# Optimization experiments

Measured on AMD Instinct MI355X. Metric: run time of the kernel, lower is better.

Reference implementation:

```python
import jax, jax.numpy as jnp
import numpy as np

B = 32768
STATE, BELIEF, HID, EMB, ACT = 100, 200, 200, 1024, 32
MIN_STD = 0.1

def _dense_init(key, fan_in, fan_out):
    k1, k2 = jax.random.split(key)
    scale = 1.0 / np.sqrt(fan_in)
    W = jax.random.uniform(k1, (fan_in, fan_out), jnp.float32, -scale, scale)
    b = jnp.zeros((fan_out,), jnp.float32)
    return W, b

def setup_inputs() -> dict:
    key = jax.random.key(0)
    ks = jax.random.split(key, 20)
    inp = {
        'prev_state': jax.random.normal(ks[0], (1, B, STATE), jnp.float32),
        'prev_action': jax.random.normal(ks[1], (1, B, ACT), jnp.float32),
        'prev_belief': jax.random.normal(ks[2], (1, B, BELIEF), jnp.float32),
        'observation': jax.random.normal(ks[3], (1, B, EMB), jnp.float32),
        'nonterminals': jnp.ones((1, B, 1), jnp.float32),
    }
    # fc_embed_state_action: (state+action) -> belief_dim, relu
    inp['W_sa'], inp['b_sa'] = _dense_init(ks[4], STATE + ACT, BELIEF)
    # GRUCell: carry = hidden (belief_dim), inputs = prev_belief (belief_dim)
    inp['W_ir'], inp['b_ir'] = _dense_init(ks[5], BELIEF, BELIEF)
    inp['W_iz'], inp['b_iz'] = _dense_init(ks[6], BELIEF, BELIEF)
    inp['W_in'], inp['b_in'] = _dense_init(ks[7], BELIEF, BELIEF)
    inp['W_hr'], _ = _dense_init(ks[8], BELIEF, BELIEF)   # no bias (flax GRUCell)
    inp['W_hz'], _ = _dense_init(ks[9], BELIEF, BELIEF)   # no bias
    inp['W_hn'], inp['b_hn'] = _dense_init(ks[10], BELIEF, BELIEF)
    # prior head
    inp['W_bp'], inp['b_bp'] = _dense_init(ks[11], BELIEF, HID)
    inp['W_sp'], inp['b_sp'] = _dense_init(ks[12], HID, 2 * STATE)
    # posterior head
    inp['W_bq'], inp['b_bq'] = _dense_init(ks[13], BELIEF + EMB, HID)
    inp['W_sq'], inp['b_sq'] = _dense_init(ks[14], HID, 2 * STATE)
    return inp

def reference(prev_state, prev_action, prev_belief, observation, nonterminals,
              W_sa, b_sa, W_ir, b_ir, W_iz, b_iz, W_in, b_in,
              W_hr, W_hz, W_hn, b_hn,
              W_bp, b_bp, W_sp, b_sp, W_bq, b_bq, W_sq, b_sq):
    noise_key = jax.random.key(42)  # stands in for the module's fixed self.rng
    s = prev_state * nonterminals  # broadcast mask over last dim
    # fc_embed_state_action (relu, activate_final=True)
    h = jax.nn.relu(jnp.concatenate([s, prev_action], axis=-1) @ W_sa + b_sa)
    # flax GRUCell with carry = h, inputs = prev_belief
    x = prev_belief
    r = jax.nn.sigmoid(x @ W_ir + b_ir + h @ W_hr)
    z = jax.nn.sigmoid(x @ W_iz + b_iz + h @ W_hz)
    n = jnp.tanh(x @ W_in + b_in + r * (h @ W_hn + b_hn))
    new_belief = (1.0 - z) * n + z * h
    # prior
    hp = jax.nn.relu(new_belief @ W_bp + b_bp)
    prior_out = jax.nn.relu(hp @ W_sp + b_sp)  # activate_final=True
    prior_mean, prior_std_raw = jnp.split(prior_out, 2, axis=-1)
    prior_std = jax.nn.softplus(prior_std_raw) + MIN_STD
    eps = jax.random.normal(noise_key, prior_mean.shape, prior_mean.dtype)
    prior_state = prior_mean + prior_std * eps
    # posterior
    hq = jax.nn.relu(jnp.concatenate([new_belief, observation], axis=-1) @ W_bq + b_bq)
    post_out = jax.nn.relu(hq @ W_sq + b_sq)
    post_mean, post_std_raw = jnp.split(post_out, 2, axis=-1)
    post_std = jax.nn.softplus(post_std_raw) + MIN_STD
    eps2 = jax.random.normal(noise_key, post_mean.shape, post_mean.dtype)  # same rng reused, as in source
    post_state = post_mean + post_std * eps2
    return (new_belief, prior_state, prior_mean, prior_std, post_state, post_mean, post_std)
```

## Files before the change

### kernel.cpp

```cpp
#include <hip/hip_runtime.h>
#include <stdint.h>

typedef short short8 __attribute__((ext_vector_type(8)));
typedef float floatx4 __attribute__((ext_vector_type(4)));
typedef unsigned short ushort_t;

#define BATCH 32768
#define STR   232
#define SLAB  (16*STR)
#define TOT_TILES 1391

#define M_SA 0
#define M_IR 1
#define M_HR 2
#define M_IZ 3
#define M_HZ 4
#define M_IN 5
#define M_HN 6
#define M_BP 7
#define M_SP 8
#define M_SQ 9
#define M_BQ 10

__device__ constexpr int TILE0[11] = {0,65,156,247,338,429,520,611,702,793,884};
__device__ constexpr int KLIM[11]  = {132,200,200,200,200,200,200,200,200,200,0};

__device__ __forceinline__ ushort_t f2bf(float f){
  uint32_t u = __float_as_uint(f);
  uint32_t r = (u + 0x7fffu + ((u >> 16) & 1u)) >> 16;
  return (ushort_t)r;
}
__device__ __forceinline__ float bf2f(ushort_t h){ return __uint_as_float(((uint32_t)h) << 16); }

__device__ __forceinline__ float sigmf_(float x){ return 1.f / (1.f + expf(-x)); }
__device__ __forceinline__ float softplusf_(float x){
  return fmaxf(x, 0.f) + log1pf(expf(-fabsf(x)));
}
__device__ __forceinline__ uint32_t rotl32(uint32_t x, int r){ return (x << r) | (x >> (32 - r)); }

__device__ __forceinline__ void threefry2x32_k42(uint32_t x0, uint32_t x1,
                                                 uint32_t& o0, uint32_t& o1){
  const uint32_t k0 = 0u, k1 = 42u, k2 = 0u ^ 42u ^ 0x1BD11BDAu;
  x0 += k0; x1 += k1;
#define TF_R(rot) { x0 += x1; x1 = rotl32(x1, rot); x1 ^= x0; }
  TF_R(13) TF_R(15) TF_R(26) TF_R(6)  x0 += k1; x1 += k2 + 1u;
  TF_R(17) TF_R(29) TF_R(16) TF_R(24) x0 += k2; x1 += k0 + 2u;
  TF_R(13) TF_R(15) TF_R(26) TF_R(6)  x0 += k0; x1 += k1 + 3u;
  TF_R(17) TF_R(29) TF_R(16) TF_R(24) x0 += k1; x1 += k2 + 4u;
  TF_R(13) TF_R(15) TF_R(26) TF_R(6)  x0 += k2; x1 += k0 + 5u;
#undef TF_R
  o0 = x0; o1 = x1;
}

__device__ __forceinline__ float jax_erfinv(float x){
  float w = -log1pf(-x * x);
  float p;
  if (w < 5.0f) {
    w -= 2.5f;
    p = 2.81022636e-08f;
    p = fmaf(p, w, 3.43273939e-07f);
    p = fmaf(p, w, -3.5233877e-06f);
    p = fmaf(p, w, -4.39150654e-06f);
    p = fmaf(p, w, 0.00021858087f);
    p = fmaf(p, w, -0.00125372503f);
    p = fmaf(p, w, -0.00417768164f);
    p = fmaf(p, w, 0.246640727f);
    p = fmaf(p, w, 1.50140941f);
  } else {
    w = sqrtf(w) - 3.0f;
    p = -0.000200214257f;
    p = fmaf(p, w, 0.000100950558f);
    p = fmaf(p, w, 0.00134934322f);
    p = fmaf(p, w, -0.00367342844f);
    p = fmaf(p, w, 0.00573950773f);
    p = fmaf(p, w, -0.0076224613f);
    p = fmaf(p, w, 0.00943887047f);
    p = fmaf(p, w, 1.00167406f);
    p = fmaf(p, w, 2.83297682f);
  }
  return p * x;
}

__device__ __forceinline__ float jax_normal_at(uint32_t j){
  uint32_t o0, o1;
  threefry2x32_k42(0u, j, o0, o1);
  uint32_t bits = o0 ^ o1;
  const float lo = -0.99999994f;
  float f = __uint_as_float((bits >> 9) | 0x3f800000u) - 1.0f;
  float fm = f * 1.99999994f;
  float u = fmaxf(lo, fm + lo);
  return 1.41421356f * jax_erfinv(u);
}

struct ConvP { const float* src[11]; ushort_t* dst; };

__global__ void __launch_bounds__(64) convw(ConvP cp)
{
  int t = blockIdx.x;
  int lane = threadIdx.x;
  const int cum[12] = {0,65,156,247,338,429,520,611,702,793,884,1391};
  int mi = 0;
  #pragma unroll
  for (int i = 0; i < 11; ++i) if (t >= cum[i+1]) mi = i+1;
  int lt = t - cum[mi];
  int kb = lt / 13, nt = lt - kb*13;
  const float* S = cp.src[mi];
  int q = lane >> 4, m = lane & 15;
  int n = nt*16 + m;
  ushort_t* D = cp.dst + (size_t)t*512 + lane*8;
  #pragma unroll
  for (int j = 0; j < 8; ++j){
    int k = kb*32 + q*8 + j;
    float v = 0.f;
    if (n < 200){
      if (mi == 10){
        if (k < 200) v = S[k*200+n];
        else if (k >= 224) v = S[(size_t)(k-24)*200+n];
      } else {
        int K = (mi == 0) ? 132 : 200;
        if (k < K) v = S[k*200+n];
      }
    }
    D[j] = f2bf(v);
  }
}

struct MainP {
  const float* prev_state; const float* prev_action; const float* prev_belief;
  const float* observation; const float* nonterm;
  const float* b_sa; const float* b_ir; const float* b_iz; const float* b_in; const float* b_hn;
  const float* b_bp; const float* b_sp; const float* b_bq; const float* b_sq;
  const float* W[11];
  const ushort_t* ws;
  float* out;
};

__device__ __forceinline__ short8 afrag(const ushort_t* buf, int m, int kb, int q){
  return *(const short8*)(buf + m*STR + kb*32 + q*8);
}

#define NSTEPS 214
#define STAGE_US 3584

struct Sched {
  short t0[NSTEPS]; signed char cnt[NSTEPS];
  constexpr Sched() : t0(), cnt() {
    int s = 0;
    for (int kb = 0; kb < 5; ++kb){
      t0[s] = (short)(0 + kb*13);     cnt[s] = 7; ++s;
      t0[s] = (short)(0 + kb*13 + 7); cnt[s] = 6; ++s;
    }
    for (int kb = 0; kb < 7; ++kb)
      for (int mt = 1; mt <= 6; ++mt){ t0[s] = (short)(65 + 91*(mt-1) + kb*13);     cnt[s] = 7; ++s; }
    for (int kb = 0; kb < 7; ++kb)
      for (int mt = 1; mt <= 6; ++mt){ t0[s] = (short)(65 + 91*(mt-1) + kb*13 + 7); cnt[s] = 6; ++s; }
    for (int kb = 0; kb < 7; ++kb){
      t0[s] = (short)(611 + kb*13);     cnt[s] = 7; ++s;
      t0[s] = (short)(611 + kb*13 + 7); cnt[s] = 6; ++s;
    }
    for (int kb = 0; kb < 7; ++kb){
      t0[s] = (short)(702 + kb*13);     cnt[s] = 7; ++s;
      t0[s] = (short)(702 + kb*13 + 7); cnt[s] = 6; ++s;
    }
    for (int kb = 0; kb < 39; ++kb){
      t0[s] = (short)(884 + kb*13);     cnt[s] = 7; ++s;
      t0[s] = (short)(884 + kb*13 + 7); cnt[s] = 6; ++s;
    }
    for (int kb = 0; kb < 7; ++kb){
      t0[s] = (short)(793 + kb*13);     cnt[s] = 7; ++s;
      t0[s] = (short)(793 + kb*13 + 7); cnt[s] = 6; ++s;
    }
  }
};
__device__ constexpr Sched SCHED{};

__device__ __forceinline__ void stage_issue(const ushort_t* ws, ushort_t* sbuf,
                                            int step, int w, int lane)
{
  if (step >= NSTEPS) return;
  const int t0 = SCHED.t0[step];
  const int cn = SCHED.cnt[step];
  ushort_t* dstb = sbuf + (step & 1) * STAGE_US;
  const ushort_t* srcb = ws + ((size_t)t0 << 9) + (lane << 3);
  #pragma unroll
  for (int r = 0; r < 2; ++r){
    int tt = w + r*4;
    if (tt < cn){
      __builtin_amdgcn_global_load_lds(
        (const __attribute__((address_space(1))) uint32_t*)(const void*)(srcb + (tt << 9)),
        (__attribute__((address_space(3)))       uint32_t*)(void*)(dstb + (tt << 9)),
        16, 0, 0);
    }
  }
}

__device__ __forceinline__ short8 sfrag(const ushort_t* sbuf, int step, int j, int lane){
  return *(const short8*)(sbuf + (step & 1) * STAGE_US + (j << 9) + (lane << 3));
}

__device__ __forceinline__ void gemm13_kb(const MainP& p, ushort_t* stageb, int& sidx,
    const ushort_t* asrc, floatx4 (&acc)[13], int kb, int m, int q, int lane, int w)
{
  short8 a = afrag(asrc, m, kb, q);
  stage_issue(p.ws, stageb, sidx+1, w, lane);
  #pragma unroll
  for (int j = 0; j < 7; ++j)
    acc[j] = __builtin_amdgcn_mfma_f32_16x16x32_bf16(a, sfrag(stageb, sidx, j, lane), acc[j], 0,0,0);
  __syncthreads(); ++sidx;
  stage_issue(p.ws, stageb, sidx+1, w, lane);
  #pragma unroll
  for (int j = 0; j < 6; ++j)
    acc[7+j] = __builtin_amdgcn_mfma_f32_16x16x32_bf16(a, sfrag(stageb, sidx, j, lane), acc[7+j], 0,0,0);
  __syncthreads(); ++sidx;
}

template<int CNT, int NT0>
__device__ __forceinline__ void gru_chunk_staged(const MainP& p, ushort_t* stageb, int& sidx,
    const ushort_t* bufX, const ushort_t* bufH, int R0, int m, int q, int lane, int w,
    floatx4 (&nbv)[13])
{
  floatx4 aR[CNT], aZ[CNT], aXN[CNT], aHN[CNT];
  #pragma unroll
  for (int i = 0; i < CNT; ++i){
    int col = (NT0+i)*16 + m;
    float br = (col<200)? p.b_ir[col] : 0.f;
    float bz = (col<200)? p.b_iz[col] : 0.f;
    float bn = (col<200)? p.b_in[col] : 0.f;
    float bh = (col<200)? p.b_hn[col] : 0.f;
    aR[i]  = (floatx4){br,br,br,br};
    aZ[i]  = (floatx4){bz,bz,bz,bz};
    aXN[i] = (floatx4){bn,bn,bn,bn};
    aHN[i] = (floatx4){bh,bh,bh,bh};
  }
#define GRU_STEP(AV, ACC) \
  stage_issue(p.ws, stageb, sidx+1, w, lane); \
  _Pragma("unroll") \
  for (int i = 0; i < CNT; ++i) \
    ACC[i] = __builtin_amdgcn_mfma_f32_16x16x32_bf16(AV, sfrag(stageb, sidx, i, lane), ACC[i], 0,0,0); \
  __syncthreads(); ++sidx;

  #pragma unroll 1
  for (int kb = 0; kb < 7; ++kb){
    short8 ax = afrag(bufX, m, kb, q);
    short8 ah = afrag(bufH, m, kb, q);
    GRU_STEP(ax, aR)
    GRU_STEP(ah, aR)
    GRU_STEP(ax, aZ)
    GRU_STEP(ah, aZ)
    GRU_STEP(ax, aXN)
    GRU_STEP(ah, aHN)
  }
#undef GRU_STEP
  #pragma unroll
  for (int i = 0; i < CNT; ++i){
    int col = (NT0+i)*16 + m;
    if (col < 200){
      #pragma unroll
      for (int rg = 0; rg < 4; ++rg){
        int rowl = q*4 + rg;
        float rr = sigmf_(aR[i][rg]);
        float zz = sigmf_(aZ[i][rg]);
        float nn = tanhf(fmaf(rr, aHN[i][rg], aXN[i][rg]));
        float hv = bf2f(bufH[rowl*STR + col]);
        float nb = fmaf(zz, hv - nn, nn);
        nbv[NT0+i][rg] = nb;
        __builtin_nontemporal_store(nb, &p.out[(size_t)(R0+rowl)*200 + col]);
      }
    }
  }
}

__device__ __forceinline__ void head_out(const floatx4* acc, float* sdb,
    float* o_state, float* o_mean, float* o_std, int R0, int m, int q)
{
  #pragma unroll
  for (int nt = 6; nt < 13; ++nt){
    int col = nt*16 + m;
    if (col >= 100 && col < 200){
      #pragma unroll
      for (int rg = 0; rg < 4; ++rg){
        int rowl = q*4 + rg;
        float sr = fmaxf(acc[nt][rg], 0.f);
        float sd = softplusf_(sr) + 0.1f;
        sdb[rowl*100 + (col-100)] = sd;
        __builtin_nontemporal_store(sd, &o_std[(size_t)(R0+rowl)*100 + (col-100)]);
      }
    }
  }
  __syncthreads();
  #pragma unroll
  for (int nt = 0; nt < 7; ++nt){
    int col = nt*16 + m;
    if (col < 100){
      #pragma unroll
      for (int rg = 0; rg < 4; ++rg){
        int rowl = q*4 + rg;
        float mean = fmaxf(acc[nt][rg], 0.f);
        float sd = sdb[rowl*100 + col];
        float e = jax_normal_at((uint32_t)(R0+rowl)*100u + (uint32_t)col);
        __builtin_nontemporal_store(mean, &o_mean[(size_t)(R0+rowl)*100 + col]);
        __builtin_nontemporal_store(fmaf(sd, e, mean), &o_state[(size_t)(R0+rowl)*100 + col]);
      }
    }
  }
  __syncthreads();
}

__global__ void __launch_bounds__(256, 2) rssm_staged(MainP p)
{
  __shared__ __align__(16) ushort_t lds[8*SLAB + 2*STAGE_US];

  const int tid  = threadIdx.x;
  const int w    = tid >> 6;
  const int lane = tid & 63;
  const int q    = lane >> 4;
  const int m    = lane & 15;
  const int R0   = blockIdx.x * 64 + w * 16;

  ushort_t* bufX   = lds + w * 2 * SLAB;
  ushort_t* bufH   = bufX + SLAB;
  ushort_t* stageb = lds + 8*SLAB;
  int sidx = 0;

  stage_issue(p.ws, stageb, 0, w, lane);

  for (int t = lane; t < 16*160; t += 64){
    int rr = t / 160, cc = t - rr*160;
    int grow = R0 + rr;
    float v = 0.f;
    if (cc < 100)      v = p.prev_state[(size_t)grow*100 + cc] * p.nonterm[grow];
    else if (cc < 132) v = p.prev_action[(size_t)grow*32 + (cc-100)];
    bufX[rr*STR + cc] = f2bf(v);
  }
  for (int t = lane; t < 16*24; t += 64){
    int rr = t / 24, cc = 200 + (t - rr*24);
    bufH[rr*STR + cc] = 0;
  }
  __syncthreads();

  {
    floatx4 acc[13];
    #pragma unroll
    for (int nt = 0; nt < 13; ++nt){
      int col = nt*16 + m;
      float bv = (col<200)? p.b_sa[col] : 0.f;
      acc[nt] = (floatx4){bv,bv,bv,bv};
    }
    #pragma unroll 1
    for (int kb = 0; kb < 5; ++kb)
      gemm13_kb(p, stageb, sidx, bufX, acc, kb, m, q, lane, w);
    #pragma unroll
    for (int nt = 0; nt < 13; ++nt){
      int col = nt*16 + m;
      if (col < 200){
        #pragma unroll
        for (int rg = 0; rg < 4; ++rg)
          bufH[(q*4+rg)*STR + col] = f2bf(fmaxf(acc[nt][rg], 0.f));
      }
    }
  }

  for (int t = lane; t < 16*224; t += 64){
    int rr = t / 224, cc = t - rr*224;
    float v = 0.f;
    if (cc < 200)
      v = __builtin_nontemporal_load(&p.prev_belief[(size_t)(R0+rr)*200 + cc]);
    bufX[rr*STR + cc] = f2bf(v);
  }
  __syncthreads();

  floatx4 nbv[13];
  gru_chunk_staged<7,0>(p, stageb, sidx, bufX, bufH, R0, m, q, lane, w, nbv);
  gru_chunk_staged<6,7>(p, stageb, sidx, bufX, bufH, R0, m, q, lane, w, nbv);

  #pragma unroll
  for (int nt = 0; nt < 13; ++nt){
    int col = nt*16 + m;
    if (col < 200){
      #pragma unroll
      for (int rg = 0; rg < 4; ++rg)
        bufX[(q*4+rg)*STR + col] = f2bf(nbv[nt][rg]);
    }
  }

  {
    floatx4 acc[13];
    #pragma unroll
    for (int nt = 0; nt < 13; ++nt){
      int col = nt*16 + m;
      float bv = (col<200)? p.b_bp[col] : 0.f;
      acc[nt] = (floatx4){bv,bv,bv,bv};
    }
    #pragma unroll 1
    for (int kb = 0; kb < 7; ++kb)
      gemm13_kb(p, stageb, sidx, bufX, acc, kb, m, q, lane, w);
    #pragma unroll
    for (int nt = 0; nt < 13; ++nt){
      int col = nt*16 + m;
      if (col < 200){
        #pragma unroll
        for (int rg = 0; rg < 4; ++rg)
          bufH[(q*4+rg)*STR + col] = f2bf(fmaxf(acc[nt][rg], 0.f));
      }
    }
  }
  __syncthreads();

  {
    floatx4 acc[13];
    #pragma unroll
    for (int nt = 0; nt < 13; ++nt){
      int col = nt*16 + m;
      float bv = (col<200)? p.b_sp[col] : 0.f;
      acc[nt] = (floatx4){bv,bv,bv,bv};
    }
    #pragma unroll 1
    for (int kb = 0; kb < 7; ++kb)
      gemm13_kb(p, stageb, sidx, bufH, acc, kb, m, q, lane, w);
    head_out(acc, (float*)bufH,
             p.out + (size_t)BATCH*200, p.out + (size_t)BATCH*300, p.out + (size_t)BATCH*400,
             R0, m, q);
  }

  {
    floatx4 acc[13];
    #pragma unroll
    for (int nt = 0; nt < 13; ++nt){
      int col = nt*16 + m;
      float bv = (col<200)? p.b_bq[col] : 0.f;
      acc[nt] = (floatx4){bv,bv,bv,bv};
    }
    #pragma unroll 1
    for (int kb = 0; kb < 7; ++kb)
      gemm13_kb(p, stageb, sidx, bufX, acc, kb, m, q, lane, w);

    const float* orow_base = p.observation + (size_t)(R0+m)*1024;
    floatx4 o1 = __builtin_nontemporal_load((const floatx4*)(orow_base + 0 + q*8));
    floatx4 o2 = __builtin_nontemporal_load((const floatx4*)(orow_base + 0 + q*8 + 4));
    #pragma unroll 1
    for (int kb = 7; kb < 39; ++kb){
      floatx4 n1 = {0,0,0,0}, n2 = {0,0,0,0};
      if (kb < 38){
        const float* nr = orow_base + ((kb+1)*32 - 224) + q*8;
        n1 = __builtin_nontemporal_load((const floatx4*)(nr));
        n2 = __builtin_nontemporal_load((const floatx4*)(nr + 4));
      }
      short8 ao;
      ao[0] = (short)f2bf(o1[0]); ao[1] = (short)f2bf(o1[1]);
      ao[2] = (short)f2bf(o1[2]); ao[3] = (short)f2bf(o1[3]);
      ao[4] = (short)f2bf(o2[0]); ao[5] = (short)f2bf(o2[1]);
      ao[6] = (short)f2bf(o2[2]); ao[7] = (short)f2bf(o2[3]);
      stage_issue(p.ws, stageb, sidx+1, w, lane);
      #pragma unroll
      for (int j = 0; j < 7; ++j)
        acc[j] = __builtin_amdgcn_mfma_f32_16x16x32_bf16(ao, sfrag(stageb, sidx, j, lane), acc[j], 0,0,0);
      __syncthreads(); ++sidx;
      stage_issue(p.ws, stageb, sidx+1, w, lane);
      #pragma unroll
      for (int j = 0; j < 6; ++j)
        acc[7+j] = __builtin_amdgcn_mfma_f32_16x16x32_bf16(ao, sfrag(stageb, sidx, j, lane), acc[7+j], 0,0,0);
      __syncthreads(); ++sidx;
      o1 = n1; o2 = n2;
    }
    #pragma unroll
    for (int nt = 0; nt < 13; ++nt){
      int col = nt*16 + m;
      if (col < 200){
        #pragma unroll
        for (int rg = 0; rg < 4; ++rg)
          bufH[(q*4+rg)*STR + col] = f2bf(fmaxf(acc[nt][rg], 0.f));
      }
    }
    for (int t = lane; t < 16*24; t += 64){
      int rr = t / 24, cc = 200 + (t - rr*24);
      bufH[rr*STR + cc] = 0;
    }
  }
  __syncthreads();

  {
    floatx4 acc[13];
    #pragma unroll
    for (int nt = 0; nt < 13; ++nt){
      int col = nt*16 + m;
      float bv = (col<200)? p.b_sq[col] : 0.f;
      acc[nt] = (floatx4){bv,bv,bv,bv};
    }
    #pragma unroll 1
    for (int kb = 0; kb < 7; ++kb)
      gemm13_kb(p, stageb, sidx, bufH, acc, kb, m, q, lane, w);
    head_out(acc, (float*)bufX,
             p.out + (size_t)BATCH*500, p.out + (size_t)BATCH*600, p.out + (size_t)BATCH*700,
             R0, m, q);
  }
}

template<int MAT>
__device__ __forceinline__ short8 bfr0(const MainP& p, int kb, int nt, int lane, int q, int m){
  int n = nt*16 + m;
  const float* S = p.W[MAT];
  uint32_t u[8];
  #pragma unroll
  for (int j = 0; j < 8; ++j){
    int k = kb*32 + q*8 + j;
    int srow;
    if (MAT == M_BQ) srow = (k < 200) ? k : ((k >= 224) ? k - 24 : -1);
    else             srow = (k < KLIM[MAT]) ? k : -1;
    float v = (srow >= 0 && n < 200) ? S[(size_t)srow*200 + n] : 0.f;
    u[j] = __float_as_uint(v);
  }
  short8 r;
  #pragma unroll
  for (int j = 0; j < 8; ++j) r[j] = (short)(u[j] >> 16);
  return r;
}

template<int CNT, int NT0>
__device__ __forceinline__ void gru_chunk0(const MainP& p,
    const ushort_t* bufX, const ushort_t* bufH, int R0, int m, int q, int lane,
    floatx4 (&nbv)[13])
{
  floatx4 aR[CNT], aZ[CNT], aXN[CNT], aHN[CNT];
  #pragma unroll
  for (int i = 0; i < CNT; ++i){
    int col = (NT0+i)*16 + m;
    float br = (col<200)? p.b_ir[col] : 0.f;
    float bz = (col<200)? p.b_iz[col] : 0.f;
    float bn = (col<200)? p.b_in[col] : 0.f;
    float bh = (col<200)? p.b_hn[col] : 0.f;
    aR[i]  = (floatx4){br,br,br,br};
    aZ[i]  = (floatx4){bz,bz,bz,bz};
    aXN[i] = (floatx4){bn,bn,bn,bn};
    aHN[i] = (floatx4){bh,bh,bh,bh};
  }
  #pragma unroll 1
  for (int kb = 0; kb < 7; ++kb){
    short8 ax = afrag(bufX, m, kb, q);
    short8 ah = afrag(bufH, m, kb, q);
    #pragma unroll
    for (int i = 0; i < CNT; ++i){
      int nt = NT0 + i;
      aR[i]  = __builtin_amdgcn_mfma_f32_16x16x32_bf16(ax, bfr0<M_IR>(p,kb,nt,lane,q,m), aR[i], 0,0,0);
      aR[i]  = __builtin_amdgcn_mfma_f32_16x16x32_bf16(ah, bfr0<M_HR>(p,kb,nt,lane,q,m), aR[i], 0,0,0);
      aZ[i]  = __builtin_amdgcn_mfma_f32_16x16x32_bf16(ax, bfr0<M_IZ>(p,kb,nt,lane,q,m), aZ[i], 0,0,0);
      aZ[i]  = __builtin_amdgcn_mfma_f32_16x16x32_bf16(ah, bfr0<M_HZ>(p,kb,nt,lane,q,m), aZ[i], 0,0,0);
      aXN[i] = __builtin_amdgcn_mfma_f32_16x16x32_bf16(ax, bfr0<M_IN>(p,kb,nt,lane,q,m), aXN[i], 0,0,0);
      aHN[i] = __builtin_amdgcn_mfma_f32_16x16x32_bf16(ah, bfr0<M_HN>(p,kb,nt,lane,q,m), aHN[i], 0,0,0);
    }
  }
  #pragma unroll
  for (int i = 0; i < CNT; ++i){
    int col = (NT0+i)*16 + m;
    if (col < 200){
      #pragma unroll
      for (int rg = 0; rg < 4; ++rg){
        int rowl = q*4 + rg;
        float rr = sigmf_(aR[i][rg]);
        float zz = sigmf_(aZ[i][rg]);
        float nn = tanhf(fmaf(rr, aHN[i][rg], aXN[i][rg]));
        float hv = bf2f(bufH[rowl*STR + col]);
        float nb = fmaf(zz, hv - nn, nn);
        nbv[NT0+i][rg] = nb;
        __builtin_nontemporal_store(nb, &p.out[(size_t)(R0+rowl)*200 + col]);
      }
    }
  }
}

__global__ void __launch_bounds__(256, 2) rssm_direct(MainP p)
{
  __shared__ __align__(16) ushort_t lds[4 * 2 * SLAB];

  const int tid  = threadIdx.x;
  const int w    = tid >> 6;
  const int lane = tid & 63;
  const int q    = lane >> 4;
  const int m    = lane & 15;
  const int R0   = blockIdx.x * 64 + w * 16;

  ushort_t* bufX = lds + w * 2 * SLAB;
  ushort_t* bufH = bufX + SLAB;

  for (int t = lane; t < 16*160; t += 64){
    int rr = t / 160, cc = t - rr*160;
    int grow = R0 + rr;
    float v = 0.f;
    if (cc < 100)      v = p.prev_state[(size_t)grow*100 + cc] * p.nonterm[grow];
    else if (cc < 132) v = p.prev_action[(size_t)grow*32 + (cc-100)];
    bufX[rr*STR + cc] = f2bf(v);
  }
  for (int t = lane; t < 16*24; t += 64){
    int rr = t / 24, cc = 200 + (t - rr*24);
    bufH[rr*STR + cc] = 0;
  }
  __syncthreads();

  {
    floatx4 acc[13];
    #pragma unroll
    for (int nt = 0; nt < 13; ++nt){
      int col = nt*16 + m;
      float bv = (col<200)? p.b_sa[col] : 0.f;
      acc[nt] = (floatx4){bv,bv,bv,bv};
    }
    #pragma unroll 1
    for (int kb = 0; kb < 5; ++kb){
      short8 a = afrag(bufX, m, kb, q);
      #pragma unroll
      for (int nt = 0; nt < 13; ++nt)
        acc[nt] = __builtin_amdgcn_mfma_f32_16x16x32_bf16(a, bfr0<M_SA>(p,kb,nt,lane,q,m), acc[nt], 0,0,0);
    }
    #pragma unroll
    for (int nt = 0; nt < 13; ++nt){
      int col = nt*16 + m;
      if (col < 200){
        #pragma unroll
        for (int rg = 0; rg < 4; ++rg)
          bufH[(q*4+rg)*STR + col] = f2bf(fmaxf(acc[nt][rg], 0.f));
      }
    }
  }

  for (int t = lane; t < 16*224; t += 64){
    int rr = t / 224, cc = t - rr*224;
    float v = 0.f;
    if (cc < 200)
      v = __builtin_nontemporal_load(&p.prev_belief[(size_t)(R0+rr)*200 + cc]);
    bufX[rr*STR + cc] = f2bf(v);
  }
  __syncthreads();

  floatx4 nbv[13];
  gru_chunk0<7,0>(p, bufX, bufH, R0, m, q, lane, nbv);
  gru_chunk0<6,7>(p, bufX, bufH, R0, m, q, lane, nbv);

  #pragma unroll
  for (int nt = 0; nt < 13; ++nt){
    int col = nt*16 + m;
    if (col < 200){
      #pragma unroll
      for (int rg = 0; rg < 4; ++rg)
        bufX[(q*4+rg)*STR + col] = f2bf(nbv[nt][rg]);
    }
  }

  {
    floatx4 acc[13];
    #pragma unroll
    for (int nt = 0; nt < 13; ++nt){
      int col = nt*16 + m;
      float bv = (col<200)? p.b_bp[col] : 0.f;
      acc[nt] = (floatx4){bv,bv,bv,bv};
    }
    #pragma unroll 1
    for (int kb = 0; kb < 7; ++kb){
      short8 a = afrag(bufX, m, kb, q);
      #pragma unroll
      for (int nt = 0; nt < 13; ++nt)
        acc[nt] = __builtin_amdgcn_mfma_f32_16x16x32_bf16(a, bfr0<M_BP>(p,kb,nt,lane,q,m), acc[nt], 0,0,0);
    }
    #pragma unroll
    for (int nt = 0; nt < 13; ++nt){
      int col = nt*16 + m;
      if (col < 200){
        #pragma unroll
        for (int rg = 0; rg < 4; ++rg)
          bufH[(q*4+rg)*STR + col] = f2bf(fmaxf(acc[nt][rg], 0.f));
      }
    }
  }
  __syncthreads();

  {
    floatx4 acc[13];
    #pragma unroll
    for (int nt = 0; nt < 13; ++nt){
      int col = nt*16 + m;
      float bv = (col<200)? p.b_sp[col] : 0.f;
      acc[nt] = (floatx4){bv,bv,bv,bv};
    }
    #pragma unroll 1
    for (int kb = 0; kb < 7; ++kb){
      short8 a = afrag(bufH, m, kb, q);
      #pragma unroll
      for (int nt = 0; nt < 13; ++nt)
        acc[nt] = __builtin_amdgcn_mfma_f32_16x16x32_bf16(a, bfr0<M_SP>(p,kb,nt,lane,q,m), acc[nt], 0,0,0);
    }
    head_out(acc, (float*)bufH,
             p.out + (size_t)BATCH*200, p.out + (size_t)BATCH*300, p.out + (size_t)BATCH*400,
             R0, m, q);
  }

  {
    floatx4 acc[13];
    #pragma unroll
    for (int nt = 0; nt < 13; ++nt){
      int col = nt*16 + m;
      float bv = (col<200)? p.b_bq[col] : 0.f;
      acc[nt] = (floatx4){bv,bv,bv,bv};
    }
    #pragma unroll 1
    for (int kb = 0; kb < 7; ++kb){
      short8 a = afrag(bufX, m, kb, q);
      #pragma unroll
      for (int nt = 0; nt < 13; ++nt)
        acc[nt] = __builtin_amdgcn_mfma_f32_16x16x32_bf16(a, bfr0<M_BQ>(p,kb,nt,lane,q,m), acc[nt], 0,0,0);
    }
    const float* orow_base = p.observation + (size_t)(R0+m)*1024;
    #pragma unroll 1
    for (int kb = 7; kb < 39; ++kb){
      const float* orow = orow_base + (kb*32 - 224) + q*8;
      floatx4 o1 = __builtin_nontemporal_load((const floatx4*)(orow));
      floatx4 o2 = __builtin_nontemporal_load((const floatx4*)(orow + 4));
      short8 ao;
      ao[0] = (short)f2bf(o1[0]); ao[1] = (short)f2bf(o1[1]);
      ao[2] = (short)f2bf(o1[2]); ao[3] = (short)f2bf(o1[3]);
      ao[4] = (short)f2bf(o2[0]); ao[5] = (short)f2bf(o2[1]);
      ao[6] = (short)f2bf(o2[2]); ao[7] = (short)f2bf(o2[3]);
      #pragma unroll
      for (int nt = 0; nt < 13; ++nt)
        acc[nt] = __builtin_amdgcn_mfma_f32_16x16x32_bf16(ao, bfr0<M_BQ>(p,kb,nt,lane,q,m), acc[nt], 0,0,0);
    }
    #pragma unroll
    for (int nt = 0; nt < 13; ++nt){
      int col = nt*16 + m;
      if (col < 200){
        #pragma unroll
        for (int rg = 0; rg < 4; ++rg)
          bufH[(q*4+rg)*STR + col] = f2bf(fmaxf(acc[nt][rg], 0.f));
      }
    }
    for (int t = lane; t < 16*24; t += 64){
      int rr = t / 24, cc = 200 + (t - rr*24);
      bufH[rr*STR + cc] = 0;
    }
  }
  __syncthreads();

  {
    floatx4 acc[13];
    #pragma unroll
    for (int nt = 0; nt < 13; ++nt){
      int col = nt*16 + m;
      float bv = (col<200)? p.b_sq[col] : 0.f;
      acc[nt] = (floatx4){bv,bv,bv,bv};
    }
    #pragma unroll 1
    for (int kb = 0; kb < 7; ++kb){
      short8 a = afrag(bufH, m, kb, q);
      #pragma unroll
      for (int nt = 0; nt < 13; ++nt)
        acc[nt] = __builtin_amdgcn_mfma_f32_16x16x32_bf16(a, bfr0<M_SQ>(p,kb,nt,lane,q,m), acc[nt], 0,0,0);
    }
    head_out(acc, (float*)bufX,
             p.out + (size_t)BATCH*500, p.out + (size_t)BATCH*600, p.out + (size_t)BATCH*700,
             R0, m, q);
  }
}

extern "C" void kernel_launch(void* const* d_in, const int* in_sizes, int n_in,
                              void* d_out, int out_size, void* d_ws, size_t ws_size,
                              hipStream_t stream)
{
  MainP p;
  p.prev_state  = (const float*)d_in[0];
  p.prev_action = (const float*)d_in[1];
  p.prev_belief = (const float*)d_in[2];
  p.observation = (const float*)d_in[3];
  p.nonterm     = (const float*)d_in[4];
  p.b_sa = (const float*)d_in[6];
  p.b_ir = (const float*)d_in[8];
  p.b_iz = (const float*)d_in[10];
  p.b_in = (const float*)d_in[12];
  p.b_hn = (const float*)d_in[16];
  p.b_bp = (const float*)d_in[18];
  p.b_sp = (const float*)d_in[20];
  p.b_bq = (const float*)d_in[22];
  p.b_sq = (const float*)d_in[24];
  p.W[M_SA] = (const float*)d_in[5];
  p.W[M_IR] = (const float*)d_in[7];
  p.W[M_HR] = (const float*)d_in[13];
  p.W[M_IZ] = (const float*)d_in[9];
  p.W[M_HZ] = (const float*)d_in[14];
  p.W[M_IN] = (const float*)d_in[11];
  p.W[M_HN] = (const float*)d_in[15];
  p.W[M_BP] = (const float*)d_in[17];
  p.W[M_SP] = (const float*)d_in[19];
  p.W[M_SQ] = (const float*)d_in[23];
  p.W[M_BQ] = (const float*)d_in[21];
  p.ws   = (const ushort_t*)d_ws;
  p.out  = (float*)d_out;

  bool use_ws = (ws_size >= (size_t)TOT_TILES * 1024u);
  if (use_ws){
    ConvP cp;
    cp.src[0]  = p.W[M_SA]; cp.src[1]  = p.W[M_IR]; cp.src[2]  = p.W[M_HR];
    cp.src[3]  = p.W[M_IZ]; cp.src[4]  = p.W[M_HZ]; cp.src[5]  = p.W[M_IN];
    cp.src[6]  = p.W[M_HN]; cp.src[7]  = p.W[M_BP]; cp.src[8]  = p.W[M_SP];
    cp.src[9]  = p.W[M_SQ]; cp.src[10] = p.W[M_BQ];
    cp.dst     = (ushort_t*)d_ws;
    convw<<<TOT_TILES, 64, 0, stream>>>(cp);
    rssm_staged<<<512, 256, 0, stream>>>(p);
  } else {
    rssm_direct<<<512, 256, 0, stream>>>(p);
  }
}
```

Before: 525.5 us.

## Triple-buffer weight staging with partial vmcnt waits instead of full barriers

Moves the LDS weight staging ring from double to triple buffering, prefetching two steps ahead. Each full __syncthreads is replaced with an s_waitcnt vmcnt(N) that waits only for the oldest outstanding loads, followed by s_barrier, so newer prefetches and observation loads stay in flight. Several standalone barriers between phases are removed on the assumption that the next step_sync covers them. This grows LDS use, which may limit the two-blocks-per-CU occupancy, and relies on precise vmcnt accounting, so the removed barriers risk read/write races.

```diff
diff --git a/kernel.cpp b/kernel.cpp
--- a/kernel.cpp
+++ b/kernel.cpp
@@ -180,7 +180,7 @@
   if (step >= NSTEPS) return;
   const int t0 = SCHED.t0[step];
   const int cn = SCHED.cnt[step];
-  ushort_t* dstb = sbuf + (step & 1) * STAGE_US;
+  ushort_t* dstb = sbuf + (step % 3) * STAGE_US;
   const ushort_t* srcb = ws + ((size_t)t0 << 9) + (lane << 3);
   #pragma unroll
   for (int r = 0; r < 2; ++r){
@@ -195,23 +195,41 @@
 }
 
 __device__ __forceinline__ short8 sfrag(const ushort_t* sbuf, int step, int j, int lane){
-  return *(const short8*)(sbuf + (step & 1) * STAGE_US + (j << 9) + (lane << 3));
+  return *(const short8*)(sbuf + (step % 3) * STAGE_US + (j << 9) + (lane << 3));
+}
+
+__device__ __forceinline__ void step_sync(int sidx, int w, int extra)
+{
+  int n2 = 0;
+  if (sidx + 2 < NSTEPS){
+    int cn = SCHED.cnt[sidx + 2];
+    n2 = (w < cn ? 1 : 0) + ((w + 4) < cn ? 1 : 0);
+  }
+  int nw = n2 + extra;
+  switch (nw){
+    case 0:  asm volatile("s_waitcnt vmcnt(0)" ::: "memory"); break;
+    case 1:  asm volatile("s_waitcnt vmcnt(1)" ::: "memory"); break;
+    case 2:  asm volatile("s_waitcnt vmcnt(2)" ::: "memory"); break;
+    case 3:  asm volatile("s_waitcnt vmcnt(3)" ::: "memory"); break;
+    default: asm volatile("s_waitcnt vmcnt(4)" ::: "memory"); break;
+  }
+  __builtin_amdgcn_s_barrier();
 }
 
 __device__ __forceinline__ void gemm13_kb(const MainP& p, ushort_t* stageb, int& sidx,
     const ushort_t* asrc, floatx4 (&acc)[13], int kb, int m, int q, int lane, int w)
 {
   short8 a = afrag(asrc, m, kb, q);
-  stage_issue(p.ws, stageb, sidx+1, w, lane);
+  stage_issue(p.ws, stageb, sidx+2, w, lane);
   #pragma unroll
   for (int j = 0; j < 7; ++j)
     acc[j] = __builtin_amdgcn_mfma_f32_16x16x32_bf16(a, sfrag(stageb, sidx, j, lane), acc[j], 0,0,0);
-  __syncthreads(); ++sidx;
-  stage_issue(p.ws, stageb, sidx+1, w, lane);
+  step_sync(sidx, w, 0); ++sidx;
+  stage_issue(p.ws, stageb, sidx+2, w, lane);
   #pragma unroll
   for (int j = 0; j < 6; ++j)
     acc[7+j] = __builtin_amdgcn_mfma_f32_16x16x32_bf16(a, sfrag(stageb, sidx, j, lane), acc[7+j], 0,0,0);
-  __syncthreads(); ++sidx;
+  step_sync(sidx, w, 0); ++sidx;
 }
 
 template<int CNT, int NT0>
@@ -233,11 +251,11 @@
     aHN[i] = (floatx4){bh,bh,bh,bh};
   }
 #define GRU_STEP(AV, ACC) \
-  stage_issue(p.ws, stageb, sidx+1, w, lane); \
+  stage_issue(p.ws, stageb, sidx+2, w, lane); \
   _Pragma("unroll") \
   for (int i = 0; i < CNT; ++i) \
     ACC[i] = __builtin_amdgcn_mfma_f32_16x16x32_bf16(AV, sfrag(stageb, sidx, i, lane), ACC[i], 0,0,0); \
-  __syncthreads(); ++sidx;
+  step_sync(sidx, w, 0); ++sidx;
 
   #pragma unroll 1
   for (int kb = 0; kb < 7; ++kb){
@@ -287,7 +305,6 @@
       }
     }
   }
-  __syncthreads();
   #pragma unroll
   for (int nt = 0; nt < 7; ++nt){
     int col = nt*16 + m;
@@ -303,12 +320,11 @@
       }
     }
   }
-  __syncthreads();
 }
 
 __global__ void __launch_bounds__(256, 2) rssm_staged(MainP p)
 {
-  __shared__ __align__(16) ushort_t lds[8*SLAB + 2*STAGE_US];
+  __shared__ __align__(16) ushort_t lds[8*SLAB + 3*STAGE_US];
 
   const int tid  = threadIdx.x;
   const int w    = tid >> 6;
@@ -323,6 +339,7 @@
   int sidx = 0;
 
   stage_issue(p.ws, stageb, 0, w, lane);
+  stage_issue(p.ws, stageb, 1, w, lane);
 
   for (int t = lane; t < 16*160; t += 64){
     int rr = t / 160, cc = t - rr*160;
@@ -336,7 +353,8 @@
     int rr = t / 24, cc = 200 + (t - rr*24);
     bufH[rr*STR + cc] = 0;
   }
-  __syncthreads();
+  asm volatile("s_waitcnt vmcnt(0)" ::: "memory");
+  __builtin_amdgcn_s_barrier();
 
   {
     floatx4 acc[13];
@@ -367,7 +385,6 @@
       v = __builtin_nontemporal_load(&p.prev_belief[(size_t)(R0+rr)*200 + cc]);
     bufX[rr*STR + cc] = f2bf(v);
   }
-  __syncthreads();
 
   floatx4 nbv[13];
   gru_chunk_staged<7,0>(p, stageb, sidx, bufX, bufH, R0, m, q, lane, w, nbv);
@@ -404,7 +421,6 @@
       }
     }
   }
-  __syncthreads();
 
   {
     floatx4 acc[13];
@@ -435,32 +451,35 @@
       gemm13_kb(p, stageb, sidx, bufX, acc, kb, m, q, lane, w);
 
     const float* orow_base = p.observation + (size_t)(R0+m)*1024;
-    floatx4 o1 = __builtin_nontemporal_load((const floatx4*)(orow_base + 0 + q*8));
-    floatx4 o2 = __builtin_nontemporal_load((const floatx4*)(orow_base + 0 + q*8 + 4));
+    floatx4 o1 = __builtin_nontemporal_load((const floatx4*)(orow_base + q*8));
+    floatx4 o2 = __builtin_nontemporal_load((const floatx4*)(orow_base + q*8 + 4));
     #pragma unroll 1
     for (int kb = 7; kb < 39; ++kb){
-      floatx4 n1 = {0,0,0,0}, n2 = {0,0,0,0};
-      if (kb < 38){
-        const float* nr = orow_base + ((kb+1)*32 - 224) + q*8;
-        n1 = __builtin_nontemporal_load((const floatx4*)(nr));
-        n2 = __builtin_nontemporal_load((const floatx4*)(nr + 4));
-      }
       short8 ao;
       ao[0] = (short)f2bf(o1[0]); ao[1] = (short)f2bf(o1[1]);
       ao[2] = (short)f2bf(o1[2]); ao[3] = (short)f2bf(o1[3]);
       ao[4] = (short)f2bf(o2[0]); ao[5] = (short)f2bf(o2[1]);
       ao[6] = (short)f2bf(o2[2]); ao[7] = (short)f2bf(o2[3]);
-      stage_issue(p.ws, stageb, sidx+1, w, lane);
+      stage_issue(p.ws, stageb, sidx+2, w, lane);
       #pragma unroll
       for (int j = 0; j < 7; ++j)
         acc[j] = __builtin_amdgcn_mfma_f32_16x16x32_bf16(ao, sfrag(stageb, sidx, j, lane), acc[j], 0,0,0);
-      __syncthreads(); ++sidx;
-      stage_issue(p.ws, stageb, sidx+1, w, lane);
+      step_sync(sidx, w, 0); ++sidx;
+      floatx4 nn1 = {0,0,0,0}, nn2 = {0,0,0,0};
+      int ex = 0;
+      if (kb < 38){
+        const float* nr = orow_base + ((kb+1)*32 - 224) + q*8;
+        nn1 = __builtin_nontemporal_load((const floatx4*)(nr));
+        nn2 = __builtin_nontemporal_load((const floatx4*)(nr + 4));
+        ex = 2;
+      }
+      __builtin_amdgcn_sched_barrier(0);
+      stage_issue(p.ws, stageb, sidx+2, w, lane);
       #pragma unroll
       for (int j = 0; j < 6; ++j)
         acc[7+j] = __builtin_amdgcn_mfma_f32_16x16x32_bf16(ao, sfrag(stageb, sidx, j, lane), acc[7+j], 0,0,0);
-      __syncthreads(); ++sidx;
-      o1 = n1; o2 = n2;
+      step_sync(sidx, w, ex); ++sidx;
+      o1 = nn1; o2 = nn2;
     }
     #pragma unroll
     for (int nt = 0; nt < 13; ++nt){
@@ -476,7 +495,6 @@
       bufH[rr*STR + cc] = 0;
     }
   }
-  __syncthreads();
 
   {
     floatx4 acc[13];
@@ -690,6 +708,7 @@
              p.out + (size_t)BATCH*200, p.out + (size_t)BATCH*300, p.out + (size_t)BATCH*400,
              R0, m, q);
   }
+  __syncthreads();
 
   {
     floatx4 acc[13];
```

Result: faster. 513.9 us (-2.2%).
